# Optimization experiments

Measured on AMD Instinct MI355X. Metric: run time of the kernel, lower is better.

Reference implementation:

```python
import jax, jax.numpy as jnp
import numpy as np

H = 8  # num_heads


def _ln(x, g, b):
    mu = x.mean(-1, keepdims=True)
    var = ((x - mu) ** 2).mean(-1, keepdims=True)
    return (x - mu) * jax.lax.rsqrt(var + 1e-5) * g + b


def setup_inputs() -> dict:
    key = jax.random.key(0)
    ks = jax.random.split(key, 24)
    B, N, V, E, D, R, L = 8, 512, 50000, 300, 256, 100, 4
    dh = D // H
    s = 0.02
    inp = {}
    inp['token_ids'] = jax.random.randint(ks[0], (B, N), 0, V, dtype=jnp.int32)
    inp['relations'] = jax.random.randint(ks[1], (B, N, N), 0, R, dtype=jnp.int32)
    m = jax.random.bernoulli(ks[2], 0.9, (B, N, N))
    eye = jnp.eye(N, dtype=bool)[None]
    inp['relations_mask'] = jnp.logical_or(m, eye)  # keep diagonal valid so every row attends somewhere
    inp['embed'] = jax.random.normal(ks[3], (V, E), jnp.float32) * s
    inp['W_in'] = jax.random.normal(ks[4], (E, D), jnp.float32) * s
    inp['b_in'] = jnp.zeros((D,), jnp.float32)
    inp['Wq'] = jax.random.normal(ks[5], (L, D, D), jnp.float32) * s
    inp['Wk'] = jax.random.normal(ks[6], (L, D, D), jnp.float32) * s
    inp['Wv'] = jax.random.normal(ks[7], (L, D, D), jnp.float32) * s
    inp['Wo'] = jax.random.normal(ks[8], (L, D, D), jnp.float32) * s
    inp['ln1_g'] = jnp.ones((L, D), jnp.float32)
    inp['ln1_b'] = jnp.zeros((L, D), jnp.float32)
    inp['ln2_g'] = jnp.ones((L, D), jnp.float32)
    inp['ln2_b'] = jnp.zeros((L, D), jnp.float32)
    inp['W1'] = jax.random.normal(ks[9], (L, D, 4 * D), jnp.float32) * s
    inp['b1'] = jnp.zeros((L, 4 * D), jnp.float32)
    inp['W2'] = jax.random.normal(ks[10], (L, 4 * D, D), jnp.float32) * s
    inp['b2'] = jnp.zeros((L, D), jnp.float32)
    inp['rel_k_emb'] = jax.random.normal(ks[11], (R, dh), jnp.float32) * s
    inp['rel_v_emb'] = jax.random.normal(ks[12], (R, dh), jnp.float32) * s
    inp['W_out'] = jax.random.normal(ks[13], (D, D), jnp.float32) * s
    inp['b_out'] = jnp.zeros((D,), jnp.float32)
    return inp


def reference(token_ids, relations, relations_mask, embed, W_in, b_in, Wq, Wk, Wv, Wo,
              ln1_g, ln1_b, ln2_g, ln2_b, W1, b1, W2, b2, rel_k_emb, rel_v_emb, W_out, b_out):
    # Input layer: embedding lookup + projection to gnn hidden size.
    x = embed[token_ids]                          # [B,N,E]
    x = jax.nn.relu(x @ W_in + b_in)              # [B,N,D]
    B, N, D = x.shape
    dh = D // H
    # Shared relation embeddings (share_layers=True, share_heads=True): gathered once.
    rk = rel_k_emb[relations]                     # [B,N,N,dh]
    rv = rel_v_emb[relations]                     # [B,N,N,dh]
    neg = jnp.asarray(-1e9, x.dtype)
    scale = jnp.asarray(1.0 / np.sqrt(dh), x.dtype)
    L = Wq.shape[0]
    for l in range(L):  # fixed small layer count
        q = (x @ Wq[l]).reshape(B, N, H, dh).transpose(0, 2, 1, 3)
        k = (x @ Wk[l]).reshape(B, N, H, dh).transpose(0, 2, 1, 3)
        v = (x @ Wv[l]).reshape(B, N, H, dh).transpose(0, 2, 1, 3)
        # Relation-aware scores: q.k + q.r_k (RAT-SQL)
        scores = (jnp.einsum('bhnd,bhmd->bhnm', q, k)
                  + jnp.einsum('bhnd,bnmd->bhnm', q, rk)) * scale
        scores = jnp.where(relations_mask[:, None], scores, neg)
        a = jax.nn.softmax(scores, axis=-1)       # [B,H,N,N]
        z = (jnp.einsum('bhnm,bhmd->bhnd', a, v)
             + jnp.einsum('bhnm,bnmd->bhnd', a, rv))
        z = z.transpose(0, 2, 1, 3).reshape(B, N, D) @ Wo[l]
        x = _ln(x + z, ln1_g[l], ln1_b[l])
        f = jax.nn.relu(x @ W1[l] + b1[l]) @ W2[l] + b2[l]
        x = _ln(x + f, ln2_g[l], ln2_b[l])
    # Output layer projection
    return x @ W_out + b_out
```

## Files before the change

kernel.cpp:

```cpp
#include <hip/hip_runtime.h>
#include <hip/hip_bf16.h>

#define NTOK 4096
#define NN   512

typedef __attribute__((ext_vector_type(8))) short bf16x8;
typedef __attribute__((ext_vector_type(4))) float f32x4;
typedef __attribute__((ext_vector_type(4))) unsigned short u16x4;

__device__ __forceinline__ float bf16_to_f(unsigned short u) {
    unsigned int x = ((unsigned int)u) << 16;
    return __builtin_bit_cast(float, x);
}
__device__ __forceinline__ unsigned short f_to_bf16(float f) {
    unsigned int b = __builtin_bit_cast(unsigned int, f);
    return (unsigned short)((b + 0x7fff + ((b >> 16) & 1)) >> 16);
}
__device__ __forceinline__ bf16x8 pack8(float4 a, float4 b) {
    bf16x8 v;
    v[0]=(short)f_to_bf16(a.x); v[1]=(short)f_to_bf16(a.y);
    v[2]=(short)f_to_bf16(a.z); v[3]=(short)f_to_bf16(a.w);
    v[4]=(short)f_to_bf16(b.x); v[5]=(short)f_to_bf16(b.y);
    v[6]=(short)f_to_bf16(b.z); v[7]=(short)f_to_bf16(b.w);
    return v;
}

__global__ void detect_mask_kernel(const unsigned char* __restrict__ m, int* __restrict__ flag) {
    __shared__ int f;
    if (threadIdx.x == 0) f = 0;
    __syncthreads();
    int any = 0;
    for (int i = threadIdx.x; i < 4096; i += 256) {
        if ((i & 3) != 0 && m[i] != 0) any = 1;
    }
    if (any) atomicOr(&f, 1);
    __syncthreads();
    if (threadIdx.x == 0) *flag = f;
}

__global__ __launch_bounds__(256) void prep_rel16(
    const int* __restrict__ rel, const void* __restrict__ mask,
    const int* __restrict__ flag, short* __restrict__ rel16)
{
    const bool mbyte = (*flag != 0);
    const unsigned char* m8 = (const unsigned char*)mask;
    const int* m32 = (const int*)mask;
    const int i = (blockIdx.x * 256 + threadIdx.x) * 2;
    int2 rv = *(const int2*)(rel + i);
    int ok0, ok1;
    if (mbyte) { ok0 = m8[i]; ok1 = m8[i + 1]; }
    else       { ok0 = (m32[i] != 0); ok1 = (m32[i + 1] != 0); }
    short2 o;
    o.x = ok0 ? (short)rv.x : (short)-1;
    o.y = ok1 ? (short)rv.y : (short)-1;
    *(short2*)(rel16 + i) = o;
}

__global__ __launch_bounds__(256) void tcast256(
    const float* __restrict__ Wq, const float* __restrict__ Wk,
    const float* __restrict__ Wv, const float* __restrict__ Wo,
    const float* __restrict__ Wout, unsigned short* __restrict__ wt,
    int nL, float scale)
{
    const int z = blockIdx.z;
    const float* src; unsigned short* dst; float sc = 1.f;
    if (z >= nL * 4) {
        src = Wout; dst = wt + (size_t)nL * 786432;
    } else {
        const int l = z >> 2, which = z & 3;
        if      (which == 0) { src = Wq + (size_t)l * 65536; sc = scale; }
        else if (which == 1) { src = Wk + (size_t)l * 65536; }
        else if (which == 2) { src = Wv + (size_t)l * 65536; }
        else                 { src = Wo + (size_t)l * 65536; }
        dst = wt + (size_t)l * 786432 + which * 65536;
    }
    __shared__ float tile[32][33];
    const int t = threadIdx.x, tx = t & 31, ty = t >> 5;
    const int n0 = blockIdx.x * 32, k0 = blockIdx.y * 32;
#pragma unroll
    for (int p = 0; p < 4; ++p)
        tile[ty + p * 8][tx] = src[(size_t)(k0 + ty + p * 8) * 256 + n0 + tx];
    __syncthreads();
#pragma unroll
    for (int p = 0; p < 4; ++p)
        dst[(size_t)(n0 + ty + p * 8) * 256 + k0 + tx] = f_to_bf16(tile[tx][ty + p * 8] * sc);
}

__global__ __launch_bounds__(256) void tcastKN(
    const float* __restrict__ in, unsigned short* __restrict__ out,
    int K, int N, long inStride, long outStride)
{
    in  += (size_t)blockIdx.z * inStride;
    out += (size_t)blockIdx.z * outStride;
    __shared__ float tile[32][33];
    const int t = threadIdx.x, tx = t & 31, ty = t >> 5;
    const int n0 = blockIdx.x * 32, k0 = blockIdx.y * 32;
#pragma unroll
    for (int p = 0; p < 4; ++p)
        tile[ty + p * 8][tx] = in[(size_t)(k0 + ty + p * 8) * N + n0 + tx];
    __syncthreads();
#pragma unroll
    for (int p = 0; p < 4; ++p)
        out[(size_t)(n0 + ty + p * 8) * K + k0 + tx] = f_to_bf16(tile[tx][ty + p * 8]);
}

__global__ __launch_bounds__(256) void embed_proj_kernel(
    const int* __restrict__ tok, const float* __restrict__ embed,
    const float* __restrict__ W_in, const float* __restrict__ b_in,
    float* __restrict__ x, unsigned short* __restrict__ xh)
{
    __shared__ float emb[8][304];
    __shared__ int tloc[8];
    const int t = threadIdx.x;
    const int r0 = blockIdx.x * 8;
    if (t < 8) tloc[t] = tok[r0 + t];
    __syncthreads();
    for (int i = t; i < 8 * 300; i += 256) {
        int r = i / 300, e = i - r * 300;
        emb[r][e] = embed[(size_t)tloc[r] * 300 + e];
    }
    __syncthreads();
    float acc[8] = {0.f,0.f,0.f,0.f,0.f,0.f,0.f,0.f};
    const int d = t;
    for (int e = 0; e < 300; ++e) {
        float w = W_in[e * 256 + d];
#pragma unroll
        for (int r = 0; r < 8; ++r) acc[r] += emb[r][e] * w;
    }
    const float bb = b_in[d];
#pragma unroll
    for (int r = 0; r < 8; ++r) {
        float o = acc[r] + bb;
        o = o > 0.f ? o : 0.f;
        x[(size_t)(r0 + r) * 256 + d] = o;
        xh[(size_t)(r0 + r) * 256 + d] = f_to_bf16(o);
    }
}

__global__ __launch_bounds__(256) void gemm_bf16_64(
    const unsigned short* __restrict__ A, const unsigned short* __restrict__ WT,
    const float* __restrict__ bias, float* __restrict__ Cf, unsigned short* __restrict__ Ch,
    int M, int K, int Nc, int relu)
{
    __shared__ unsigned short As[2][64][40];
    __shared__ unsigned short Bs[2][64][40];
    const int t = threadIdx.x;
    const int lane = t & 63, w = t >> 6;
    const int g = lane >> 4, li = lane & 15;
    const int r0 = blockIdx.y * 64, c0 = blockIdx.x * 64;

    f32x4 acc[4];
#pragma unroll
    for (int i = 0; i < 4; ++i) acc[i] = (f32x4){0.f,0.f,0.f,0.f};

    const int arow = t >> 2, ad8 = (t & 3) * 8;

    bf16x8 a0 = *(const bf16x8*)(A  + (size_t)(r0 + arow) * K + ad8);
    bf16x8 b0 = *(const bf16x8*)(WT + (size_t)(c0 + arow) * K + ad8);

    const int nk = K >> 5;
    for (int ki = 0; ki < nk; ++ki) {
        const int cur = ki & 1;
        *(bf16x8*)&As[cur][arow][ad8] = a0;
        *(bf16x8*)&Bs[cur][arow][ad8] = b0;
        if (ki + 1 < nk) {
            const int k0 = (ki + 1) * 32;
            a0 = *(const bf16x8*)(A  + (size_t)(r0 + arow) * K + k0 + ad8);
            b0 = *(const bf16x8*)(WT + (size_t)(c0 + arow) * K + k0 + ad8);
        }
        __syncthreads();
        bf16x8 af = *(const bf16x8*)&As[cur][16 * w + li][g * 8];
#pragma unroll
        for (int sub = 0; sub < 4; ++sub) {
            bf16x8 bfr = *(const bf16x8*)&Bs[cur][16 * sub + li][g * 8];
            acc[sub] = __builtin_amdgcn_mfma_f32_16x16x32_bf16(af, bfr, acc[sub], 0, 0, 0);
        }
    }
#pragma unroll
    for (int sub = 0; sub < 4; ++sub) {
        int col = c0 + sub * 16 + li;
        float bv = bias ? bias[col] : 0.f;
#pragma unroll
        for (int r = 0; r < 4; ++r) {
            int row = r0 + 16 * w + g * 4 + r;
            float o = acc[sub][r] + bv;
            if (relu) o = fmaxf(o, 0.f);
            if (Ch) Ch[(size_t)row * Nc + col] = f_to_bf16(o);
            else    Cf[(size_t)row * Nc + col] = o;
        }
    }
}

__global__ __launch_bounds__(256) void gemm_bf16_128(
    const unsigned short* __restrict__ A, const unsigned short* __restrict__ WT,
    const float* __restrict__ bias, float* __restrict__ Cf, unsigned short* __restrict__ Ch,
    int M, int K, int Nc, int relu)
{
    __shared__ unsigned short As[2][128][40];
    __shared__ unsigned short Bs[2][64][40];
    const int t = threadIdx.x;
    const int lane = t & 63, w = t >> 6;
    const int g = lane >> 4, li = lane & 15;
    const int r0 = blockIdx.y * 128, c0 = blockIdx.x * 64;

    f32x4 acc[2][4];
#pragma unroll
    for (int i = 0; i < 2; ++i)
#pragma unroll
        for (int j = 0; j < 4; ++j) acc[i][j] = (f32x4){0.f,0.f,0.f,0.f};

    const int arow = t >> 1, ah = (t & 1) * 16;
    const int bcol = t >> 2, bk8 = (t & 3) * 8;

    bf16x8 a0 = *(const bf16x8*)(A + (size_t)(r0 + arow) * K + ah);
    bf16x8 a1 = *(const bf16x8*)(A + (size_t)(r0 + arow) * K + ah + 8);
    bf16x8 b0 = *(const bf16x8*)(WT + (size_t)(c0 + bcol) * K + bk8);

    const int nk = K >> 5;
    for (int ki = 0; ki < nk; ++ki) {
        const int cur = ki & 1;
        *(bf16x8*)&As[cur][arow][ah]     = a0;
        *(bf16x8*)&As[cur][arow][ah + 8] = a1;
        *(bf16x8*)&Bs[cur][bcol][bk8]    = b0;
        if (ki + 1 < nk) {
            const int k0 = (ki + 1) * 32;
            a0 = *(const bf16x8*)(A + (size_t)(r0 + arow) * K + k0 + ah);
            a1 = *(const bf16x8*)(A + (size_t)(r0 + arow) * K + k0 + ah + 8);
            b0 = *(const bf16x8*)(WT + (size_t)(c0 + bcol) * K + k0 + bk8);
        }
        __syncthreads();
        bf16x8 af0 = *(const bf16x8*)&As[cur][32 * w + li][g * 8];
        bf16x8 af1 = *(const bf16x8*)&As[cur][32 * w + 16 + li][g * 8];
#pragma unroll
        for (int sub = 0; sub < 4; ++sub) {
            bf16x8 bfr = *(const bf16x8*)&Bs[cur][16 * sub + li][g * 8];
            acc[0][sub] = __builtin_amdgcn_mfma_f32_16x16x32_bf16(af0, bfr, acc[0][sub], 0, 0, 0);
            acc[1][sub] = __builtin_amdgcn_mfma_f32_16x16x32_bf16(af1, bfr, acc[1][sub], 0, 0, 0);
        }
    }
#pragma unroll
    for (int rc = 0; rc < 2; ++rc)
#pragma unroll
    for (int sub = 0; sub < 4; ++sub) {
        int col = c0 + sub * 16 + li;
        float bv = bias ? bias[col] : 0.f;
#pragma unroll
        for (int r = 0; r < 4; ++r) {
            int row = r0 + 32 * w + rc * 16 + g * 4 + r;
            float o = acc[rc][sub][r] + bv;
            if (relu) o = fmaxf(o, 0.f);
            if (Ch) Ch[(size_t)row * Nc + col] = f_to_bf16(o);
            else    Cf[(size_t)row * Nc + col] = o;
        }
    }
}

__global__ __launch_bounds__(256) void qrk_kernel(
    const unsigned short* __restrict__ qkvh, const float* __restrict__ relk_g,
    unsigned short* __restrict__ qrkg)
{
    const int n0 = blockIdx.x * 64, h = blockIdx.y, b = blockIdx.z;
    const int t = threadIdx.x, lane = t & 63, w = t >> 6;
    const int g = lane >> 4, li = lane & 15;
    const int qrow = 16 * w + g * 4;

    __shared__ unsigned short relk_s[100][40];
    for (int i = t; i < 400; i += 256) {
        int rr = i >> 2, d8 = (i & 3) * 8;
        const float* sp = relk_g + rr * 32 + d8;
        *(bf16x8*)&relk_s[rr][d8] = pack8(*(const float4*)sp, *(const float4*)(sp + 4));
    }
    bf16x8 qf = *(const bf16x8*)(qkvh + (size_t)(b * NN + n0 + 16 * w + li) * 768 + h * 32 + g * 8);
    __syncthreads();
#pragma unroll
    for (int rc = 0; rc < 7; ++rc) {
        bf16x8 bb = *(const bf16x8*)&relk_s[rc * 16 + li][g * 8];
        f32x4 s = __builtin_amdgcn_mfma_f32_16x16x32_bf16(qf, bb, (f32x4){0.f,0.f,0.f,0.f}, 0, 0, 0);
        int col = rc * 16 + li;
        if (col < 100) {
#pragma unroll
            for (int r = 0; r < 4; ++r)
                qrkg[((size_t)(b * 8 + h) * NN + n0 + qrow + r) * 100 + col] = f_to_bf16(s[r]);
        }
    }
}

__global__ __launch_bounds__(256, 3) void attn_mfma(
    const unsigned short* __restrict__ qkvh,
    const short* __restrict__ rel16,
    const unsigned short* __restrict__ qrkg,
    const float* __restrict__ relv_g,
    float* __restrict__ zpart, float* __restrict__ smpart)
{
    const int p = blockIdx.x;
    const int cx = p & 7, idx0 = p >> 3;
    const int sg = cx * 8 + (idx0 >> 4);
    const int hm = idx0 & 15;
    const int h = hm >> 1, ms = hm & 1;
    const int b = sg >> 3, chunk = sg & 7;
    const int n0 = chunk * 64, mbase = ms * 256;

    const int t = threadIdx.x;
    const int lane = t & 63, w = t >> 6;
    const int g = lane >> 4, li = lane & 15;
    const int qrow = 16 * w + g * 4;

    __shared__ float wrel[64][100];
    __shared__ unsigned short qrk_lds[64][100];
    __shared__ union {
        unsigned short relvT[32][136];
        struct {
            unsigned short v_t[2][32][40];
            unsigned short p_s[4][16][40];
        } mn;
    } u;

    for (int i = t; i < 6400; i += 256) ((float*)wrel)[i] = 0.f;
    {
        const unsigned short* qsrc = qrkg + ((size_t)(b * 8 + h) * NN + n0) * 100;
        for (int i = t; i < 3200; i += 256) {
            int row = i / 50, off = (i - row * 50) * 2;
            *(unsigned int*)&qrk_lds[row][off] =
                *(const unsigned int*)(qsrc + (size_t)row * 100 + off);
        }
    }
    bf16x8 qf = *(const bf16x8*)(qkvh + (size_t)(b * NN + n0 + 16 * w + li) * 768 + h * 32 + g * 8);

    const short* relrow[4];
#pragma unroll
    for (int r = 0; r < 4; ++r)
        relrow[r] = rel16 + ((size_t)b * NN + n0 + qrow + r) * NN;
    const int vm = t & 31, vdg = t >> 5;
    const size_t kRB = (size_t)(b * NN) * 768 + 256 + h * 32 + g * 8;
    const size_t vRB = (size_t)(b * NN) * 768 + 512 + h * 32 + vdg * 4;

    bf16x8 kbuf[2][2]; u16x4 vbuf[2]; short rbuf[2][8];
#pragma unroll
    for (int i = 0; i < 8; ++i)
        rbuf[0][i] = relrow[i & 3][mbase + (i >> 2) * 16 + li];
    kbuf[0][0] = *(const bf16x8*)(qkvh + kRB + (size_t)(mbase + li) * 768);
    kbuf[0][1] = *(const bf16x8*)(qkvh + kRB + (size_t)(mbase + 16 + li) * 768);
    vbuf[0]    = *(const u16x4*)(qkvh + vRB + (size_t)(mbase + vm) * 768);

    float smacc[4] = {0.f, 0.f, 0.f, 0.f};
    f32x4 zf[2];
    zf[0] = (f32x4){0.f,0.f,0.f,0.f};
    zf[1] = (f32x4){0.f,0.f,0.f,0.f};

    __syncthreads();

#pragma unroll
    for (int tt = 0; tt < 8; ++tt) {
        const int cur = tt & 1, nxt = cur ^ 1;
        u.mn.v_t[cur][vdg * 4 + 0][vm] = vbuf[cur][0];
        u.mn.v_t[cur][vdg * 4 + 1][vm] = vbuf[cur][1];
        u.mn.v_t[cur][vdg * 4 + 2][vm] = vbuf[cur][2];
        u.mn.v_t[cur][vdg * 4 + 3][vm] = vbuf[cur][3];
        if (tt + 1 < 8) {
            const int m0n = mbase + (tt + 1) * 32;
#pragma unroll
            for (int i = 0; i < 8; ++i)
                rbuf[nxt][i] = relrow[i & 3][m0n + (i >> 2) * 16 + li];
        }
        __syncthreads();
        bf16x8 kf0 = kbuf[cur][0], kf1 = kbuf[cur][1];
        if (tt + 1 < 8) {
            const int m0n = mbase + (tt + 1) * 32;
            kbuf[nxt][0] = *(const bf16x8*)(qkvh + kRB + (size_t)(m0n + li) * 768);
            kbuf[nxt][1] = *(const bf16x8*)(qkvh + kRB + (size_t)(m0n + 16 + li) * 768);
            vbuf[nxt]    = *(const u16x4*)(qkvh + vRB + (size_t)(m0n + vm) * 768);
        }
        f32x4 s0 = __builtin_amdgcn_mfma_f32_16x16x32_bf16(qf, kf0, (f32x4){0.f,0.f,0.f,0.f}, 0, 0, 0);
        f32x4 s1 = __builtin_amdgcn_mfma_f32_16x16x32_bf16(qf, kf1, (f32x4){0.f,0.f,0.f,0.f}, 0, 0, 0);
        float pr[8];
#pragma unroll
        for (int i = 0; i < 8; ++i) {
            const int r = i & 3;
            const int rl = rbuf[cur][i];
            const float qadd = bf16_to_f(qrk_lds[qrow + r][rl < 0 ? 0 : rl]);
            const float sv = ((i >> 2) ? s1[r] : s0[r]) + qadd;
            float pv = 0.f;
            if (rl >= 0) {
                pv = __expf(fminf(sv, 50.f));
                atomicAdd(&wrel[qrow + r][rl], pv);
            }
            smacc[r] += pv;
            pr[i] = pv;
        }
#pragma unroll
        for (int i = 0; i < 8; ++i)
            u.mn.p_s[w][g * 4 + (i & 3)][(i >> 2) * 16 + li] = f_to_bf16(pr[i]);
        asm volatile("s_waitcnt lgkmcnt(0)" ::: "memory");
        __builtin_amdgcn_sched_barrier(0);
        bf16x8 pa = *(const bf16x8*)&u.mn.p_s[w][li][g * 8];
#pragma unroll
        for (int dc = 0; dc < 2; ++dc) {
            bf16x8 vb = *(const bf16x8*)&u.mn.v_t[cur][dc * 16 + li][g * 8];
            zf[dc] = __builtin_amdgcn_mfma_f32_16x16x32_bf16(pa, vb, zf[dc], 0, 0, 0);
        }
    }
    __syncthreads();

    for (int i = t; i < 32 * 36; i += 256) {
        int d = i / 36, c = 100 + (i - (i / 36) * 36);
        u.relvT[d][c] = 0;
    }
    for (int i = t; i < 400; i += 256) {
        int rr2 = i >> 2, d8 = (i & 3) * 8;
        const float* sp = relv_g + rr2 * 32 + d8;
        float4 s0 = *(const float4*)sp, s1 = *(const float4*)(sp + 4);
        u.relvT[d8 + 0][rr2] = f_to_bf16(s0.x);
        u.relvT[d8 + 1][rr2] = f_to_bf16(s0.y);
        u.relvT[d8 + 2][rr2] = f_to_bf16(s0.z);
        u.relvT[d8 + 3][rr2] = f_to_bf16(s0.w);
        u.relvT[d8 + 4][rr2] = f_to_bf16(s1.x);
        u.relvT[d8 + 5][rr2] = f_to_bf16(s1.y);
        u.relvT[d8 + 6][rr2] = f_to_bf16(s1.z);
        u.relvT[d8 + 7][rr2] = f_to_bf16(s1.w);
    }
    __syncthreads();
#pragma unroll
    for (int kc = 0; kc < 4; ++kc) {
        const int kbase = kc * 32 + g * 8;
        const float* wp = &wrel[16 * w + li][0];
        bf16x8 af;
#pragma unroll
        for (int j = 0; j < 8; ++j) {
            int id = kbase + j;
            float val = (id < 100) ? wp[id] : 0.f;
            af[j] = (short)f_to_bf16(val);
        }
#pragma unroll
        for (int dc = 0; dc < 2; ++dc) {
            bf16x8 vb = *(const bf16x8*)&u.relvT[dc * 16 + li][kbase];
            zf[dc] = __builtin_amdgcn_mfma_f32_16x16x32_bf16(af, vb, zf[dc], 0, 0, 0);
        }
    }
#pragma unroll
    for (int r = 0; r < 4; ++r) {
        smacc[r] += __shfl_xor(smacc[r], 1, 64);
        smacc[r] += __shfl_xor(smacc[r], 2, 64);
        smacc[r] += __shfl_xor(smacc[r], 4, 64);
        smacc[r] += __shfl_xor(smacc[r], 8, 64);
    }
#pragma unroll
    for (int r = 0; r < 4; ++r) {
        const int row = b * NN + n0 + qrow + r;
        size_t ob = (size_t)ms * 1048576 + (size_t)row * 256 + h * 32;
#pragma unroll
        for (int dc = 0; dc < 2; ++dc)
            zpart[ob + dc * 16 + li] = zf[dc][r];
        if (li == 0)
            smpart[(size_t)ms * 32768 + (size_t)row * 8 + h] = smacc[r];
    }
}

__global__ __launch_bounds__(256) void combine_kernel(
    const float* __restrict__ zpart, const float* __restrict__ smpart,
    unsigned short* __restrict__ zbf)
{
    const int t = threadIdx.x;
    const int wi = t >> 6, lane = t & 63;
    const int row = blockIdx.x * 4 + wi;
    const int h = lane >> 3;
    float den = 0.f;
    float4 acc = make_float4(0.f, 0.f, 0.f, 0.f);
#pragma unroll
    for (int s = 0; s < 2; ++s) {
        den += smpart[(size_t)s * 32768 + (size_t)row * 8 + h];
        float4 v = *(const float4*)(zpart + (size_t)s * 1048576 + (size_t)row * 256 + lane * 4);
        acc.x += v.x; acc.y += v.y; acc.z += v.z; acc.w += v.w;
    }
    const float inv = 1.f / den;
    u16x4 oh;
    oh[0] = f_to_bf16(acc.x * inv);
    oh[1] = f_to_bf16(acc.y * inv);
    oh[2] = f_to_bf16(acc.z * inv);
    oh[3] = f_to_bf16(acc.w * inv);
    *(u16x4*)(zbf + (size_t)row * 256 + lane * 4) = oh;
}

__global__ __launch_bounds__(256) void ln_kernel(
    const float* __restrict__ xin, const float* __restrict__ y,
    const float* __restrict__ g, const float* __restrict__ bsh,
    float* __restrict__ xout, unsigned short* __restrict__ xh)
{
    const int t = threadIdx.x;
    const int w = t >> 6, lane = t & 63;
    const size_t row = (size_t)blockIdx.x * 4 + w;
    const float4 xv = *(const float4*)(xin + row * 256 + lane * 4);
    const float4 yv = *(const float4*)(y + row * 256 + lane * 4);
    float4 sv;
    sv.x = xv.x + yv.x; sv.y = xv.y + yv.y; sv.z = xv.z + yv.z; sv.w = xv.w + yv.w;
    float sum = sv.x + sv.y + sv.z + sv.w;
    float sq  = sv.x * sv.x + sv.y * sv.y + sv.z * sv.z + sv.w * sv.w;
#pragma unroll
    for (int off = 1; off < 64; off <<= 1) {
        sum += __shfl_xor(sum, off, 64);
        sq  += __shfl_xor(sq, off, 64);
    }
    const float mu = sum * (1.f / 256.f);
    const float var = sq * (1.f / 256.f) - mu * mu;
    const float rs = rsqrtf(var + 1e-5f);
    const float4 gv = *(const float4*)(g + lane * 4);
    const float4 bv = *(const float4*)(bsh + lane * 4);
    float4 o;
    o.x = (sv.x - mu) * rs * gv.x + bv.x;
    o.y = (sv.y - mu) * rs * gv.y + bv.y;
    o.z = (sv.z - mu) * rs * gv.z + bv.z;
    o.w = (sv.w - mu) * rs * gv.w + bv.w;
    *(float4*)(xout + row * 256 + lane * 4) = o;
    u16x4 oh;
    oh[0] = f_to_bf16(o.x); oh[1] = f_to_bf16(o.y);
    oh[2] = f_to_bf16(o.z); oh[3] = f_to_bf16(o.w);
    *(u16x4*)(xh + row * 256 + lane * 4) = oh;
}

extern "C" void kernel_launch(void* const* d_in, const int* in_sizes, int n_in,
                              void* d_out, int out_size, void* d_ws, size_t ws_size,
                              hipStream_t stream)
{
    (void)in_sizes; (void)n_in; (void)out_size;
    const int*   tok   = (const int*)d_in[0];
    const int*   rel   = (const int*)d_in[1];
    const void*  mask  = d_in[2];
    const float* embed = (const float*)d_in[3];
    const float* W_in  = (const float*)d_in[4];
    const float* b_in  = (const float*)d_in[5];
    const float* Wq    = (const float*)d_in[6];
    const float* Wk    = (const float*)d_in[7];
    const float* Wv    = (const float*)d_in[8];
    const float* Wo    = (const float*)d_in[9];
    const float* ln1g  = (const float*)d_in[10];
    const float* ln1b  = (const float*)d_in[11];
    const float* ln2g  = (const float*)d_in[12];
    const float* ln2b  = (const float*)d_in[13];
    const float* W1    = (const float*)d_in[14];
    const float* b1    = (const float*)d_in[15];
    const float* W2    = (const float*)d_in[16];
    const float* b2    = (const float*)d_in[17];
    const float* relk  = (const float*)d_in[18];
    const float* relv  = (const float*)d_in[19];
    const float* Wout  = (const float*)d_in[20];
    const float* bout  = (const float*)d_in[21];
    float* out = (float*)d_out;
    const float scale = 0.17677669529663687f;

    float* ws = (float*)d_ws;
    float*          x     = ws;
    unsigned short* xh    = (unsigned short*)(ws + 1048576);
    unsigned short* zbf   = (unsigned short*)(ws + 1572864);
    float*          zo    = ws + 2097152;
    unsigned short* qkvh  = (unsigned short*)(ws + 3145728);
    unsigned short* hbh   = (unsigned short*)(ws + 4718592);
    float*          zpart = ws + 6815744;
    float*          smpart= ws + 8912896;
    unsigned short* qrkg  = (unsigned short*)(ws + 8978432);
    int*            flag  = (int*)(ws + 10616832);
    unsigned short* wt    = (unsigned short*)(ws + 10616848);

    const size_t wsf = ws_size >> 2;
    const bool tierA = wsf >= 13271100;
    short* rel16 = tierA ? (short*)(ws + 12222480) : (short*)hbh;

    detect_mask_kernel<<<1, 256, 0, stream>>>((const unsigned char*)mask, flag);
    embed_proj_kernel<<<512, 256, 0, stream>>>(tok, embed, W_in, b_in, x, xh);
    if (tierA) {
        prep_rel16<<<4096, 256, 0, stream>>>(rel, mask, flag, rel16);
        tcast256<<<dim3(8, 8, 17), 256, 0, stream>>>(Wq, Wk, Wv, Wo, Wout, wt, 4, scale);
        tcastKN<<<dim3(32, 8, 4), 256, 0, stream>>>(W1, wt + 262144, 256, 1024, 262144, 786432);
        tcastKN<<<dim3(8, 32, 4), 256, 0, stream>>>(W2, wt + 524288, 1024, 256, 262144, 786432);
    }

    for (int l = 0; l < 4; ++l) {
        unsigned short* wl = tierA ? wt + (size_t)l * 786432 : wt;
        if (!tierA) {
            prep_rel16<<<4096, 256, 0, stream>>>(rel, mask, flag, rel16);
            tcast256<<<dim3(8, 8, 4), 256, 0, stream>>>(
                Wq + (size_t)l * 65536, Wk + (size_t)l * 65536,
                Wv + (size_t)l * 65536, Wo + (size_t)l * 65536, Wout, wt, 1, scale);
            tcastKN<<<dim3(32, 8, 1), 256, 0, stream>>>(W1 + (size_t)l * 262144, wt + 262144, 256, 1024, 0, 0);
            tcastKN<<<dim3(8, 32, 1), 256, 0, stream>>>(W2 + (size_t)l * 262144, wt + 524288, 1024, 256, 0, 0);
        }
        gemm_bf16_128<<<dim3(12, 32), 256, 0, stream>>>(xh, wl, nullptr, nullptr, qkvh,
                                                        NTOK, 256, 768, 0);
        qrk_kernel<<<dim3(8, 8, 8), 256, 0, stream>>>(qkvh, relk, qrkg);
        attn_mfma<<<1024, 256, 0, stream>>>(qkvh, rel16, qrkg, relv, zpart, smpart);
        combine_kernel<<<1024, 256, 0, stream>>>(zpart, smpart, zbf);
        gemm_bf16_64<<<dim3(4, 64), 256, 0, stream>>>(zbf, wl + 196608, nullptr, zo, nullptr,
                                                      NTOK, 256, 256, 0);
        ln_kernel<<<1024, 256, 0, stream>>>(x, zo, ln1g + l * 256, ln1b + l * 256, x, xh);
        gemm_bf16_128<<<dim3(16, 32), 256, 0, stream>>>(xh, wl + 262144, b1 + l * 1024, nullptr, hbh,
                                                        NTOK, 256, 1024, 1);
        gemm_bf16_64<<<dim3(4, 64), 256, 0, stream>>>(hbh, wl + 524288, b2 + l * 256, zo, nullptr,
                                                      NTOK, 1024, 256, 0);
        ln_kernel<<<1024, 256, 0, stream>>>(x, zo, ln2g + l * 256, ln2b + l * 256, x, xh);
    }
    unsigned short* woutT = wt;
    if (tierA) {
        woutT = wt + (size_t)4 * 786432;
    } else {
        tcast256<<<dim3(8, 8, 1), 256, 0, stream>>>(Wq, Wk, Wv, Wo, Wout, wt, 0, scale);
    }
    gemm_bf16_64<<<dim3(4, 64), 256, 0, stream>>>(xh, woutT, bout, out, nullptr,
                                                  NTOK, 256, 256, 0);
}
```

Baseline: 646.8 us.

## Load V fragments directly into registers and drop per-tile block barriers

The attention kernel no longer stages V through a shared transposed buffer. Each lane gathers its own V MFMA operand straight from global memory with scalar 16-bit loads, and the zeroing of wrel and the loading of qrk_lds are made per-wave. This removes the __syncthreads in every tile iteration and at setup, so the four waves run independently. In exchange it issues many small strided global loads and raises register pressure, and the occupancy hint in launch_bounds is removed.

```diff
diff --git a/kernel.cpp b/kernel.cpp
--- a/kernel.cpp
+++ b/kernel.cpp
@@ -285,7 +285,7 @@
     }
 }
 
-__global__ __launch_bounds__(256, 3) void attn_mfma(
+__global__ __launch_bounds__(256) void attn_mfma(
     const unsigned short* __restrict__ qkvh,
     const short* __restrict__ rel16,
     const unsigned short* __restrict__ qrkg,
@@ -309,18 +309,18 @@
     __shared__ unsigned short qrk_lds[64][100];
     __shared__ union {
         unsigned short relvT[32][136];
-        struct {
-            unsigned short v_t[2][32][40];
-            unsigned short p_s[4][16][40];
-        } mn;
+        unsigned short p_s[4][16][40];
     } u;
 
-    for (int i = t; i < 6400; i += 256) ((float*)wrel)[i] = 0.f;
+    for (int i = lane; i < 1600; i += 64) {
+        int row = i / 100;
+        wrel[16 * w + row][i - row * 100] = 0.f;
+    }
     {
-        const unsigned short* qsrc = qrkg + ((size_t)(b * 8 + h) * NN + n0) * 100;
-        for (int i = t; i < 3200; i += 256) {
+        const unsigned short* qsrc = qrkg + ((size_t)(b * 8 + h) * NN + n0 + 16 * w) * 100;
+        for (int i = lane; i < 800; i += 64) {
             int row = i / 50, off = (i - row * 50) * 2;
-            *(unsigned int*)&qrk_lds[row][off] =
+            *(unsigned int*)&qrk_lds[16 * w + row][off] =
                 *(const unsigned int*)(qsrc + (size_t)row * 100 + off);
         }
     }
@@ -330,48 +330,52 @@
 #pragma unroll
     for (int r = 0; r < 4; ++r)
         relrow[r] = rel16 + ((size_t)b * NN + n0 + qrow + r) * NN;
-    const int vm = t & 31, vdg = t >> 5;
-    const size_t kRB = (size_t)(b * NN) * 768 + 256 + h * 32 + g * 8;
-    const size_t vRB = (size_t)(b * NN) * 768 + 512 + h * 32 + vdg * 4;
-
-    bf16x8 kbuf[2][2]; u16x4 vbuf[2]; short rbuf[2][8];
-#pragma unroll
-    for (int i = 0; i < 8; ++i)
-        rbuf[0][i] = relrow[i & 3][mbase + (i >> 2) * 16 + li];
-    kbuf[0][0] = *(const bf16x8*)(qkvh + kRB + (size_t)(mbase + li) * 768);
-    kbuf[0][1] = *(const bf16x8*)(qkvh + kRB + (size_t)(mbase + 16 + li) * 768);
-    vbuf[0]    = *(const u16x4*)(qkvh + vRB + (size_t)(mbase + vm) * 768);
+    const size_t kRB  = (size_t)(b * NN) * 768 + 256 + h * 32 + g * 8;
+    const size_t vRB2 = (size_t)(b * NN) * 768 + 512 + h * 32;
+
+    bf16x8 kbuf[2][2]; bf16x8 vb[2][2]; short rbuf[2][8];
+    {
+#pragma unroll
+        for (int i = 0; i < 8; ++i)
+            rbuf[0][i] = relrow[i & 3][mbase + (i >> 2) * 16 + li];
+        kbuf[0][0] = *(const bf16x8*)(qkvh + kRB + (size_t)(mbase + li) * 768);
+        kbuf[0][1] = *(const bf16x8*)(qkvh + kRB + (size_t)(mbase + 16 + li) * 768);
+#pragma unroll
+        for (int dc = 0; dc < 2; ++dc) {
+            bf16x8 v;
+#pragma unroll
+            for (int j = 0; j < 8; ++j)
+                v[j] = (short)qkvh[vRB2 + (size_t)(mbase + g * 8 + j) * 768 + dc * 16 + li];
+            vb[0][dc] = v;
+        }
+    }
 
     float smacc[4] = {0.f, 0.f, 0.f, 0.f};
     f32x4 zf[2];
     zf[0] = (f32x4){0.f,0.f,0.f,0.f};
     zf[1] = (f32x4){0.f,0.f,0.f,0.f};
 
-    __syncthreads();
-
 #pragma unroll
     for (int tt = 0; tt < 8; ++tt) {
         const int cur = tt & 1, nxt = cur ^ 1;
-        u.mn.v_t[cur][vdg * 4 + 0][vm] = vbuf[cur][0];
-        u.mn.v_t[cur][vdg * 4 + 1][vm] = vbuf[cur][1];
-        u.mn.v_t[cur][vdg * 4 + 2][vm] = vbuf[cur][2];
-        u.mn.v_t[cur][vdg * 4 + 3][vm] = vbuf[cur][3];
         if (tt + 1 < 8) {
             const int m0n = mbase + (tt + 1) * 32;
 #pragma unroll
             for (int i = 0; i < 8; ++i)
                 rbuf[nxt][i] = relrow[i & 3][m0n + (i >> 2) * 16 + li];
-        }
-        __syncthreads();
-        bf16x8 kf0 = kbuf[cur][0], kf1 = kbuf[cur][1];
-        if (tt + 1 < 8) {
-            const int m0n = mbase + (tt + 1) * 32;
             kbuf[nxt][0] = *(const bf16x8*)(qkvh + kRB + (size_t)(m0n + li) * 768);
             kbuf[nxt][1] = *(const bf16x8*)(qkvh + kRB + (size_t)(m0n + 16 + li) * 768);
-            vbuf[nxt]    = *(const u16x4*)(qkvh + vRB + (size_t)(m0n + vm) * 768);
-        }
-        f32x4 s0 = __builtin_amdgcn_mfma_f32_16x16x32_bf16(qf, kf0, (f32x4){0.f,0.f,0.f,0.f}, 0, 0, 0);
-        f32x4 s1 = __builtin_amdgcn_mfma_f32_16x16x32_bf16(qf, kf1, (f32x4){0.f,0.f,0.f,0.f}, 0, 0, 0);
+#pragma unroll
+            for (int dc = 0; dc < 2; ++dc) {
+                bf16x8 v;
+#pragma unroll
+                for (int j = 0; j < 8; ++j)
+                    v[j] = (short)qkvh[vRB2 + (size_t)(m0n + g * 8 + j) * 768 + dc * 16 + li];
+                vb[nxt][dc] = v;
+            }
+        }
+        f32x4 s0 = __builtin_amdgcn_mfma_f32_16x16x32_bf16(qf, kbuf[cur][0], (f32x4){0.f,0.f,0.f,0.f}, 0, 0, 0);
+        f32x4 s1 = __builtin_amdgcn_mfma_f32_16x16x32_bf16(qf, kbuf[cur][1], (f32x4){0.f,0.f,0.f,0.f}, 0, 0, 0);
         float pr[8];
 #pragma unroll
         for (int i = 0; i < 8; ++i) {
@@ -389,15 +393,12 @@
         }
 #pragma unroll
         for (int i = 0; i < 8; ++i)
-            u.mn.p_s[w][g * 4 + (i & 3)][(i >> 2) * 16 + li] = f_to_bf16(pr[i]);
+            u.p_s[w][g * 4 + (i & 3)][(i >> 2) * 16 + li] = f_to_bf16(pr[i]);
         asm volatile("s_waitcnt lgkmcnt(0)" ::: "memory");
         __builtin_amdgcn_sched_barrier(0);
-        bf16x8 pa = *(const bf16x8*)&u.mn.p_s[w][li][g * 8];
-#pragma unroll
-        for (int dc = 0; dc < 2; ++dc) {
-            bf16x8 vb = *(const bf16x8*)&u.mn.v_t[cur][dc * 16 + li][g * 8];
-            zf[dc] = __builtin_amdgcn_mfma_f32_16x16x32_bf16(pa, vb, zf[dc], 0, 0, 0);
-        }
+        bf16x8 pa = *(const bf16x8*)&u.p_s[w][li][g * 8];
+        zf[0] = __builtin_amdgcn_mfma_f32_16x16x32_bf16(pa, vb[cur][0], zf[0], 0, 0, 0);
+        zf[1] = __builtin_amdgcn_mfma_f32_16x16x32_bf16(pa, vb[cur][1], zf[1], 0, 0, 0);
     }
     __syncthreads();
 
@@ -432,8 +433,8 @@
         }
 #pragma unroll
         for (int dc = 0; dc < 2; ++dc) {
-            bf16x8 vb = *(const bf16x8*)&u.relvT[dc * 16 + li][kbase];
-            zf[dc] = __builtin_amdgcn_mfma_f32_16x16x32_bf16(af, vb, zf[dc], 0, 0, 0);
+            bf16x8 vbr = *(const bf16x8*)&u.relvT[dc * 16 + li][kbase];
+            zf[dc] = __builtin_amdgcn_mfma_f32_16x16x32_bf16(af, vbr, zf[dc], 0, 0, 0);
         }
     }
 #pragma unroll
```

Measured after the change: 646.6 us. No clear change (-0.0%).

## Shrink GEMM tiles and split attention key range across waves within a block

Applied to the files above, without the earlier changes.

Replaces the 128-row GEMM with a 32-row-tile variant and moves the GEMM launches to smaller tiles so more blocks fill the GPU. The attention kernel now handles 32 query rows per block, with two wave pairs each covering half of the key range. Each pair keeps its own V staging buffer, and only one pair applies the relation-value term. The goal is higher occupancy and more parallelism for this small problem, at the cost of less data reuse per block and more redundant loads. The barrier before the main loop was also removed, which risks a race on the wrel/qrk_lds setup.

```diff
diff --git a/kernel.cpp b/kernel.cpp
--- a/kernel.cpp
+++ b/kernel.cpp
@@ -191,63 +191,54 @@
     }
 }
 
-__global__ __launch_bounds__(256) void gemm_bf16_128(
+__global__ __launch_bounds__(256) void gemm_bf16_32(
     const unsigned short* __restrict__ A, const unsigned short* __restrict__ WT,
     const float* __restrict__ bias, float* __restrict__ Cf, unsigned short* __restrict__ Ch,
     int M, int K, int Nc, int relu)
 {
-    __shared__ unsigned short As[2][128][40];
+    __shared__ unsigned short As[2][32][40];
     __shared__ unsigned short Bs[2][64][40];
     const int t = threadIdx.x;
     const int lane = t & 63, w = t >> 6;
     const int g = lane >> 4, li = lane & 15;
-    const int r0 = blockIdx.y * 128, c0 = blockIdx.x * 64;
-
-    f32x4 acc[2][4];
-#pragma unroll
-    for (int i = 0; i < 2; ++i)
-#pragma unroll
-        for (int j = 0; j < 4; ++j) acc[i][j] = (f32x4){0.f,0.f,0.f,0.f};
-
-    const int arow = t >> 1, ah = (t & 1) * 16;
+    const int r0 = blockIdx.y * 32, c0 = blockIdx.x * 64;
+
+    f32x4 acc[2];
+    acc[0] = (f32x4){0.f,0.f,0.f,0.f};
+    acc[1] = (f32x4){0.f,0.f,0.f,0.f};
+
+    const int arow = t >> 3, a4 = (t & 7) * 4;
     const int bcol = t >> 2, bk8 = (t & 3) * 8;
 
-    bf16x8 a0 = *(const bf16x8*)(A + (size_t)(r0 + arow) * K + ah);
-    bf16x8 a1 = *(const bf16x8*)(A + (size_t)(r0 + arow) * K + ah + 8);
+    u16x4 a0 = *(const u16x4*)(A + (size_t)(r0 + arow) * K + a4);
     bf16x8 b0 = *(const bf16x8*)(WT + (size_t)(c0 + bcol) * K + bk8);
 
     const int nk = K >> 5;
     for (int ki = 0; ki < nk; ++ki) {
         const int cur = ki & 1;
-        *(bf16x8*)&As[cur][arow][ah]     = a0;
-        *(bf16x8*)&As[cur][arow][ah + 8] = a1;
-        *(bf16x8*)&Bs[cur][bcol][bk8]    = b0;
+        *(u16x4*)&As[cur][arow][a4] = a0;
+        *(bf16x8*)&Bs[cur][bcol][bk8] = b0;
         if (ki + 1 < nk) {
             const int k0 = (ki + 1) * 32;
-            a0 = *(const bf16x8*)(A + (size_t)(r0 + arow) * K + k0 + ah);
-            a1 = *(const bf16x8*)(A + (size_t)(r0 + arow) * K + k0 + ah + 8);
+            a0 = *(const u16x4*)(A + (size_t)(r0 + arow) * K + k0 + a4);
             b0 = *(const bf16x8*)(WT + (size_t)(c0 + bcol) * K + k0 + bk8);
         }
         __syncthreads();
-        bf16x8 af0 = *(const bf16x8*)&As[cur][32 * w + li][g * 8];
-        bf16x8 af1 = *(const bf16x8*)&As[cur][32 * w + 16 + li][g * 8];
-#pragma unroll
-        for (int sub = 0; sub < 4; ++sub) {
-            bf16x8 bfr = *(const bf16x8*)&Bs[cur][16 * sub + li][g * 8];
-            acc[0][sub] = __builtin_amdgcn_mfma_f32_16x16x32_bf16(af0, bfr, acc[0][sub], 0, 0, 0);
-            acc[1][sub] = __builtin_amdgcn_mfma_f32_16x16x32_bf16(af1, bfr, acc[1][sub], 0, 0, 0);
-        }
-    }
-#pragma unroll
-    for (int rc = 0; rc < 2; ++rc)
-#pragma unroll
-    for (int sub = 0; sub < 4; ++sub) {
-        int col = c0 + sub * 16 + li;
+        bf16x8 af = *(const bf16x8*)&As[cur][16 * (w & 1) + li][g * 8];
+#pragma unroll
+        for (int sub = 0; sub < 2; ++sub) {
+            bf16x8 bfr = *(const bf16x8*)&Bs[cur][(w >> 1) * 32 + sub * 16 + li][g * 8];
+            acc[sub] = __builtin_amdgcn_mfma_f32_16x16x32_bf16(af, bfr, acc[sub], 0, 0, 0);
+        }
+    }
+#pragma unroll
+    for (int sub = 0; sub < 2; ++sub) {
+        int col = c0 + (w >> 1) * 32 + sub * 16 + li;
         float bv = bias ? bias[col] : 0.f;
 #pragma unroll
         for (int r = 0; r < 4; ++r) {
-            int row = r0 + 32 * w + rc * 16 + g * 4 + r;
-            float o = acc[rc][sub][r] + bv;
+            int row = r0 + 16 * (w & 1) + g * 4 + r;
+            float o = acc[sub][r] + bv;
             if (relu) o = fmaxf(o, 0.f);
             if (Ch) Ch[(size_t)row * Nc + col] = f_to_bf16(o);
             else    Cf[(size_t)row * Nc + col] = o;
@@ -285,7 +276,7 @@
     }
 }
 
-__global__ __launch_bounds__(256, 3) void attn_mfma(
+__global__ __launch_bounds__(256, 4) void attn_mfma(
     const unsigned short* __restrict__ qkvh,
     const short* __restrict__ rel16,
     const unsigned short* __restrict__ qrkg,
@@ -293,69 +284,71 @@
     float* __restrict__ zpart, float* __restrict__ smpart)
 {
     const int p = blockIdx.x;
-    const int cx = p & 7, idx0 = p >> 3;
-    const int sg = cx * 8 + (idx0 >> 4);
-    const int hm = idx0 & 15;
-    const int h = hm >> 1, ms = hm & 1;
-    const int b = sg >> 3, chunk = sg & 7;
-    const int n0 = chunk * 64, mbase = ms * 256;
+    const int cx = p & 7, k = p >> 3;
+    const int sg = cx * 16 + (k >> 3);
+    const int h  = k & 7;
+    const int b = sg >> 4, chunk = sg & 15;
+    const int n0 = chunk * 32;
 
     const int t = threadIdx.x;
     const int lane = t & 63, w = t >> 6;
+    const int qw = w & 1, mhalf = w >> 1;
     const int g = lane >> 4, li = lane & 15;
-    const int qrow = 16 * w + g * 4;
-
-    __shared__ float wrel[64][100];
-    __shared__ unsigned short qrk_lds[64][100];
+    const int qrow = 16 * qw + g * 4;
+    const int mbase = mhalf * 256;
+
+    __shared__ float wrel[32][100];
+    __shared__ unsigned short qrk_lds[32][100];
     __shared__ union {
         unsigned short relvT[32][136];
         struct {
-            unsigned short v_t[2][32][40];
+            unsigned short v_t[2][2][32][40];
             unsigned short p_s[4][16][40];
         } mn;
     } u;
 
-    for (int i = t; i < 6400; i += 256) ((float*)wrel)[i] = 0.f;
+    for (int i = t; i < 3200; i += 256) ((float*)wrel)[i] = 0.f;
     {
         const unsigned short* qsrc = qrkg + ((size_t)(b * 8 + h) * NN + n0) * 100;
-        for (int i = t; i < 3200; i += 256) {
+        for (int i = t; i < 1600; i += 256) {
             int row = i / 50, off = (i - row * 50) * 2;
             *(unsigned int*)&qrk_lds[row][off] =
                 *(const unsigned int*)(qsrc + (size_t)row * 100 + off);
         }
     }
-    bf16x8 qf = *(const bf16x8*)(qkvh + (size_t)(b * NN + n0 + 16 * w + li) * 768 + h * 32 + g * 8);
+    bf16x8 qf = *(const bf16x8*)(qkvh + (size_t)(b * NN + n0 + 16 * qw + li) * 768 + h * 32 + g * 8);
 
     const short* relrow[4];
 #pragma unroll
     for (int r = 0; r < 4; ++r)
         relrow[r] = rel16 + ((size_t)b * NN + n0 + qrow + r) * NN;
-    const int vm = t & 31, vdg = t >> 5;
+    const int th = t & 127;
+    const int vm = th & 31, vdg = th >> 5;
     const size_t kRB = (size_t)(b * NN) * 768 + 256 + h * 32 + g * 8;
-    const size_t vRB = (size_t)(b * NN) * 768 + 512 + h * 32 + vdg * 4;
-
-    bf16x8 kbuf[2][2]; u16x4 vbuf[2]; short rbuf[2][8];
+    const size_t vRB = (size_t)(b * NN) * 768 + 512 + h * 32 + vdg * 8;
+
+    bf16x8 kbuf[2][2]; bf16x8 vbuf[2]; short rbuf[2][8];
 #pragma unroll
     for (int i = 0; i < 8; ++i)
         rbuf[0][i] = relrow[i & 3][mbase + (i >> 2) * 16 + li];
     kbuf[0][0] = *(const bf16x8*)(qkvh + kRB + (size_t)(mbase + li) * 768);
     kbuf[0][1] = *(const bf16x8*)(qkvh + kRB + (size_t)(mbase + 16 + li) * 768);
-    vbuf[0]    = *(const u16x4*)(qkvh + vRB + (size_t)(mbase + vm) * 768);
+    vbuf[0]    = *(const bf16x8*)(qkvh + vRB + (size_t)(mbase + vm) * 768);
 
     float smacc[4] = {0.f, 0.f, 0.f, 0.f};
     f32x4 zf[2];
     zf[0] = (f32x4){0.f,0.f,0.f,0.f};
     zf[1] = (f32x4){0.f,0.f,0.f,0.f};
 
-    __syncthreads();
-
 #pragma unroll
     for (int tt = 0; tt < 8; ++tt) {
         const int cur = tt & 1, nxt = cur ^ 1;
-        u.mn.v_t[cur][vdg * 4 + 0][vm] = vbuf[cur][0];
-        u.mn.v_t[cur][vdg * 4 + 1][vm] = vbuf[cur][1];
-        u.mn.v_t[cur][vdg * 4 + 2][vm] = vbuf[cur][2];
-        u.mn.v_t[cur][vdg * 4 + 3][vm] = vbuf[cur][3];
+        {
+            bf16x8 vv = vbuf[cur];
+#pragma unroll
+            for (int j = 0; j < 8; ++j)
+                u.mn.v_t[mhalf][cur][vdg * 8 + j][vm] = (unsigned short)vv[j];
+        }
         if (tt + 1 < 8) {
             const int m0n = mbase + (tt + 1) * 32;
 #pragma unroll
@@ -368,7 +361,7 @@
             const int m0n = mbase + (tt + 1) * 32;
             kbuf[nxt][0] = *(const bf16x8*)(qkvh + kRB + (size_t)(m0n + li) * 768);
             kbuf[nxt][1] = *(const bf16x8*)(qkvh + kRB + (size_t)(m0n + 16 + li) * 768);
-            vbuf[nxt]    = *(const u16x4*)(qkvh + vRB + (size_t)(m0n + vm) * 768);
+            vbuf[nxt]    = *(const bf16x8*)(qkvh + vRB + (size_t)(m0n + vm) * 768);
         }
         f32x4 s0 = __builtin_amdgcn_mfma_f32_16x16x32_bf16(qf, kf0, (f32x4){0.f,0.f,0.f,0.f}, 0, 0, 0);
         f32x4 s1 = __builtin_amdgcn_mfma_f32_16x16x32_bf16(qf, kf1, (f32x4){0.f,0.f,0.f,0.f}, 0, 0, 0);
@@ -395,7 +388,7 @@
         bf16x8 pa = *(const bf16x8*)&u.mn.p_s[w][li][g * 8];
 #pragma unroll
         for (int dc = 0; dc < 2; ++dc) {
-            bf16x8 vb = *(const bf16x8*)&u.mn.v_t[cur][dc * 16 + li][g * 8];
+            bf16x8 vb = *(const bf16x8*)&u.mn.v_t[mhalf][cur][dc * 16 + li][g * 8];
             zf[dc] = __builtin_amdgcn_mfma_f32_16x16x32_bf16(pa, vb, zf[dc], 0, 0, 0);
         }
     }
@@ -419,21 +412,23 @@
         u.relvT[d8 + 7][rr2] = f_to_bf16(s1.w);
     }
     __syncthreads();
-#pragma unroll
-    for (int kc = 0; kc < 4; ++kc) {
-        const int kbase = kc * 32 + g * 8;
-        const float* wp = &wrel[16 * w + li][0];
-        bf16x8 af;
-#pragma unroll
-        for (int j = 0; j < 8; ++j) {
-            int id = kbase + j;
-            float val = (id < 100) ? wp[id] : 0.f;
-            af[j] = (short)f_to_bf16(val);
-        }
-#pragma unroll
-        for (int dc = 0; dc < 2; ++dc) {
-            bf16x8 vb = *(const bf16x8*)&u.relvT[dc * 16 + li][kbase];
-            zf[dc] = __builtin_amdgcn_mfma_f32_16x16x32_bf16(af, vb, zf[dc], 0, 0, 0);
+    if (mhalf == 0) {
+#pragma unroll
+        for (int kc = 0; kc < 4; ++kc) {
+            const int kbase = kc * 32 + g * 8;
+            const float* wp = &wrel[16 * qw + li][0];
+            bf16x8 af;
+#pragma unroll
+            for (int j = 0; j < 8; ++j) {
+                int id = kbase + j;
+                float val = (id < 100) ? wp[id] : 0.f;
+                af[j] = (short)f_to_bf16(val);
+            }
+#pragma unroll
+            for (int dc = 0; dc < 2; ++dc) {
+                bf16x8 vbr = *(const bf16x8*)&u.relvT[dc * 16 + li][kbase];
+                zf[dc] = __builtin_amdgcn_mfma_f32_16x16x32_bf16(af, vbr, zf[dc], 0, 0, 0);
+            }
         }
     }
 #pragma unroll
@@ -446,12 +441,12 @@
 #pragma unroll
     for (int r = 0; r < 4; ++r) {
         const int row = b * NN + n0 + qrow + r;
-        size_t ob = (size_t)ms * 1048576 + (size_t)row * 256 + h * 32;
+        size_t ob = (size_t)mhalf * 1048576 + (size_t)row * 256 + h * 32;
 #pragma unroll
         for (int dc = 0; dc < 2; ++dc)
             zpart[ob + dc * 16 + li] = zf[dc][r];
         if (li == 0)
-            smpart[(size_t)ms * 32768 + (size_t)row * 8 + h] = smacc[r];
+            smpart[(size_t)mhalf * 32768 + (size_t)row * 8 + h] = smacc[r];
     }
 }
 
@@ -582,18 +577,18 @@
             tcastKN<<<dim3(32, 8, 1), 256, 0, stream>>>(W1 + (size_t)l * 262144, wt + 262144, 256, 1024, 0, 0);
             tcastKN<<<dim3(8, 32, 1), 256, 0, stream>>>(W2 + (size_t)l * 262144, wt + 524288, 1024, 256, 0, 0);
         }
-        gemm_bf16_128<<<dim3(12, 32), 256, 0, stream>>>(xh, wl, nullptr, nullptr, qkvh,
-                                                        NTOK, 256, 768, 0);
+        gemm_bf16_64<<<dim3(12, 64), 256, 0, stream>>>(xh, wl, nullptr, nullptr, qkvh,
+                                                       NTOK, 256, 768, 0);
         qrk_kernel<<<dim3(8, 8, 8), 256, 0, stream>>>(qkvh, relk, qrkg);
         attn_mfma<<<1024, 256, 0, stream>>>(qkvh, rel16, qrkg, relv, zpart, smpart);
         combine_kernel<<<1024, 256, 0, stream>>>(zpart, smpart, zbf);
-        gemm_bf16_64<<<dim3(4, 64), 256, 0, stream>>>(zbf, wl + 196608, nullptr, zo, nullptr,
-                                                      NTOK, 256, 256, 0);
+        gemm_bf16_32<<<dim3(4, 128), 256, 0, stream>>>(zbf, wl + 196608, nullptr, zo, nullptr,
+                                                       NTOK, 256, 256, 0);
         ln_kernel<<<1024, 256, 0, stream>>>(x, zo, ln1g + l * 256, ln1b + l * 256, x, xh);
-        gemm_bf16_128<<<dim3(16, 32), 256, 0, stream>>>(xh, wl + 262144, b1 + l * 1024, nullptr, hbh,
-                                                        NTOK, 256, 1024, 1);
-        gemm_bf16_64<<<dim3(4, 64), 256, 0, stream>>>(hbh, wl + 524288, b2 + l * 256, zo, nullptr,
-                                                      NTOK, 1024, 256, 0);
+        gemm_bf16_64<<<dim3(16, 64), 256, 0, stream>>>(xh, wl + 262144, b1 + l * 1024, nullptr, hbh,
+                                                       NTOK, 256, 1024, 1);
+        gemm_bf16_32<<<dim3(4, 128), 256, 0, stream>>>(hbh, wl + 524288, b2 + l * 256, zo, nullptr,
+                                                       NTOK, 1024, 256, 0);
         ln_kernel<<<1024, 256, 0, stream>>>(x, zo, ln2g + l * 256, ln2b + l * 256, x, xh);
     }
     unsigned short* woutT = wt;
@@ -602,6 +597,6 @@
     } else {
         tcast256<<<dim3(8, 8, 1), 256, 0, stream>>>(Wq, Wk, Wv, Wo, Wout, wt, 0, scale);
     }
-    gemm_bf16_64<<<dim3(4, 64), 256, 0, stream>>>(xh, woutT, bout, out, nullptr,
-                                                  NTOK, 256, 256, 0);
-}
+    gemm_bf16_32<<<dim3(4, 128), 256, 0, stream>>>(xh, woutT, bout, out, nullptr,
+                                                   NTOK, 256, 256, 0);
+}
```

Measured after the change: 617.3 us. -4.6%, faster.
